# Kernel optimization log

Measured on AMD Instinct MI355X. Metric: run time of the kernel, lower is better.

Reference implementation:

```python
import jax, jax.numpy as jnp
import numpy as np

B, S, D, H = 4, 2048, 512, 8
DH = D // H


def setup_inputs() -> dict:
    key = jax.random.key(0)
    ks = jax.random.split(key, 7)
    scale = 1.0 / np.sqrt(DH)  # mimic nn.Linear init magnitude
    return {
        "x": jax.random.normal(ks[0], (B, S, D), dtype=jnp.float32),
        "Wq": jax.random.normal(ks[1], (H, DH, DH), dtype=jnp.float32) * scale,
        "bq": jax.random.normal(ks[2], (H, DH), dtype=jnp.float32) * scale,
        "Wk": jax.random.normal(ks[3], (H, DH, DH), dtype=jnp.float32) * scale,
        "bk": jax.random.normal(ks[4], (H, DH), dtype=jnp.float32) * scale,
        "Wv": jax.random.normal(ks[5], (H, DH, DH), dtype=jnp.float32) * scale,
        "bv": jax.random.normal(ks[6], (H, DH), dtype=jnp.float32) * scale,
    }


def reference(x, Wq, bq, Wk, bk, Wv, bv):
    # x: [B, S, D] -> per-head slices [B, S, H, DH] (contiguous chunks, as in torch slicing)
    xh = x.reshape(B, S, H, DH)
    # nn.Linear: y = x @ W.T + b, per head. Wq[h] is [out, in].
    q = jnp.einsum("bshd,hed->bshe", xh, Wq) + bq  # [B, S, H, DH]
    k = jnp.einsum("bshd,hed->bshe", xh, Wk) + bk
    v = jnp.einsum("bshd,hed->bshe", xh, Wv) + bv
    scores = jnp.einsum("bshe,bthe->bhst", q, k) / jnp.sqrt(jnp.float32(DH))  # [B, H, S, S]
    attn = jax.nn.softmax(scores, axis=-1)
    out = jnp.einsum("bhst,bthe->bshe", attn, v)  # [B, S, H, DH]
    return out.reshape(B, S, D)  # hstack of head outputs == concat along feature dim
```

## Files before the change

### kernel.cpp

```cpp
#include <hip/hip_runtime.h>
#include <math.h>

#define B_ 4
#define S_ 2048
#define D_ 512
#define H_ 8
#define DH_ 64
#define BH_ (B_*H_)
#define SCALE 0.1803368801111243f

typedef __attribute__((ext_vector_type(4))) float f32x4;
typedef __attribute__((ext_vector_type(8))) short bf16x8;

__device__ inline uint rnepk(float a, float b) {
    uint ua = __builtin_bit_cast(uint, a), ub = __builtin_bit_cast(uint, b);
    ua += 0x7FFFu + ((ua >> 16) & 1u);
    ub += 0x7FFFu + ((ub >> 16) & 1u);
    return (ua >> 16) | (ub & 0xFFFF0000u);
}
__device__ inline uint truncpk(float lo, float hi) {
    return __builtin_amdgcn_perm(__builtin_bit_cast(uint, hi),
                                 __builtin_bit_cast(uint, lo), 0x07060302u);
}

__global__ __launch_bounds__(256)
void qkv_mfma(const float* __restrict__ x,
              const float* __restrict__ Wq, const float* __restrict__ bq,
              const float* __restrict__ Wk, const float* __restrict__ bk,
              const float* __restrict__ Wv, const float* __restrict__ bv,
              ushort* __restrict__ Qb, ushort* __restrict__ Kb,
              ushort* __restrict__ Vtg)
{
    const int bh = blockIdx.x, b = bh >> 3, h = bh & 7;
    const int s0 = blockIdx.y * 64;
    const int tid = threadIdx.x;
    const int w = tid >> 6, lane = tid & 63, la = lane & 15, lg = lane >> 4;

    __shared__ __align__(16) ushort xs[64 * 64];
    __shared__ __align__(16) ushort wl[3 * 64 * 64];

    {
        const int s = tid >> 2, ch0 = (tid & 3) * 2;
        const float* xr = x + ((size_t)(b * S_ + s0 + s)) * D_ + h * DH_ + ch0 * 8;
        float4 f0 = *(const float4*)(xr);
        float4 f1 = *(const float4*)(xr + 4);
        float4 f2 = *(const float4*)(xr + 8);
        float4 f3 = *(const float4*)(xr + 12);
        uint4 c0, c1;
        c0.x = rnepk(f0.x, f0.y); c0.y = rnepk(f0.z, f0.w);
        c0.z = rnepk(f1.x, f1.y); c0.w = rnepk(f1.z, f1.w);
        c1.x = rnepk(f2.x, f2.y); c1.y = rnepk(f2.z, f2.w);
        c1.z = rnepk(f3.x, f3.y); c1.w = rnepk(f3.z, f3.w);
        *(uint4*)(xs + s * 64 + ((ch0 ^ (s & 7)) * 8)) = c0;
        *(uint4*)(xs + s * 64 + (((ch0 + 1) ^ (s & 7)) * 8)) = c1;
    }
    {
        const float* Wm[3] = {Wq, Wk, Wv};
        #pragma unroll
        for (int it = 0; it < 6; ++it) {
            const int mat = it >> 1;
            const int e = (it & 1) * 32 + (tid >> 3);
            const int ch = tid & 7;
            const float* p = Wm[mat] + h * DH_ * DH_ + e * DH_ + ch * 8;
            float4 a = *(const float4*)(p);
            float4 bb = *(const float4*)(p + 4);
            uint4 u;
            u.x = rnepk(a.x, a.y);  u.y = rnepk(a.z, a.w);
            u.z = rnepk(bb.x, bb.y); u.w = rnepk(bb.z, bb.w);
            *(uint4*)(wl + mat * 4096 + e * 64 + ((ch ^ (e & 7)) * 8)) = u;
        }
    }
    __syncthreads();

    const int srow = w * 16 + la;
    const ushort* xrow = xs + srow * 64;
    bf16x8 xf0 = *(const bf16x8*)(xrow + ((lg ^ (la & 7)) * 8));
    bf16x8 xf1 = *(const bf16x8*)(xrow + (((4 + lg) ^ (la & 7)) * 8));

    const size_t qkbase = ((size_t)(bh * S_ + s0 + srow)) * DH_;

    #pragma unroll
    for (int t4 = 0; t4 < 4; ++t4) {
        const int er = t4 * 16 + la;
        const ushort* wqr = wl + er * 64;
        const ushort* wkr = wl + 4096 + er * 64;
        const ushort* wvr = wl + 8192 + er * 64;
        const int c0 = (lg ^ (la & 7)) * 8, c1 = ((4 + lg) ^ (la & 7)) * 8;
        bf16x8 wq0 = *(const bf16x8*)(wqr + c0), wq1 = *(const bf16x8*)(wqr + c1);
        bf16x8 wk0 = *(const bf16x8*)(wkr + c0), wk1 = *(const bf16x8*)(wkr + c1);
        bf16x8 wv0 = *(const bf16x8*)(wvr + c0), wv1 = *(const bf16x8*)(wvr + c1);

        f32x4 aq = {0.f,0.f,0.f,0.f}, ak = {0.f,0.f,0.f,0.f}, av = {0.f,0.f,0.f,0.f};
        aq = __builtin_amdgcn_mfma_f32_16x16x32_bf16(wq0, xf0, aq, 0, 0, 0);
        aq = __builtin_amdgcn_mfma_f32_16x16x32_bf16(wq1, xf1, aq, 0, 0, 0);
        ak = __builtin_amdgcn_mfma_f32_16x16x32_bf16(wk0, xf0, ak, 0, 0, 0);
        ak = __builtin_amdgcn_mfma_f32_16x16x32_bf16(wk1, xf1, ak, 0, 0, 0);
        av = __builtin_amdgcn_mfma_f32_16x16x32_bf16(xf0, wv0, av, 0, 0, 0);
        av = __builtin_amdgcn_mfma_f32_16x16x32_bf16(xf1, wv1, av, 0, 0, 0);

        float4 bq4 = *(const float4*)(bq + h * DH_ + t4 * 16 + lg * 4);
        float4 bk4 = *(const float4*)(bk + h * DH_ + t4 * 16 + lg * 4);
        float bvv = bv[h * DH_ + er];

        uint2 qo, ko, vo;
        qo.x = rnepk((aq[0] + bq4.x) * SCALE, (aq[1] + bq4.y) * SCALE);
        qo.y = rnepk((aq[2] + bq4.z) * SCALE, (aq[3] + bq4.w) * SCALE);
        ko.x = rnepk(ak[0] + bk4.x, ak[1] + bk4.y);
        ko.y = rnepk(ak[2] + bk4.z, ak[3] + bk4.w);
        vo.x = rnepk(av[0] + bvv, av[1] + bvv);
        vo.y = rnepk(av[2] + bvv, av[3] + bvv);
        *(uint2*)(Qb + qkbase + t4 * 16 + lg * 4) = qo;
        *(uint2*)(Kb + qkbase + t4 * 16 + lg * 4) = ko;
        *(uint2*)(Vtg + ((size_t)(bh * DH_ + er)) * S_ + s0 + w * 16 + lg * 4) = vo;
    }
}

__global__ __launch_bounds__(256)
void flash_mfma(const ushort* __restrict__ Qb, const ushort* __restrict__ Kb,
                const ushort* __restrict__ Vtg, float* __restrict__ out)
{
    const int blk = blockIdx.x;
    const int bh = blk >> 5, qc = blk & 31;
    const int b = bh >> 3, h = bh & 7;
    const int tid = threadIdx.x;
    const int w = tid >> 6, lane = tid & 63, la = lane & 15, lg = lane >> 4;

    __shared__ __align__(16) ushort Ks[64 * 64];
    __shared__ __align__(16) ushort Vs[64 * 64];
    __shared__ __align__(16) ushort Ps[4][16 * 72];

    const int q0 = qc * 64 + w * 16;
    const ushort* qrow = Qb + ((size_t)(bh * S_) + q0 + la) * DH_;
    bf16x8 qf0 = *(const bf16x8*)(qrow + lg * 8);
    bf16x8 qf1 = *(const bf16x8*)(qrow + 32 + lg * 8);

    f32x4 O[4];
    #pragma unroll
    for (int t4 = 0; t4 < 4; ++t4) O[t4] = (f32x4){0.f, 0.f, 0.f, 0.f};
    float lsum = 0.f;

    const int sr = tid >> 3, sch = tid & 7;
    const ushort* kq = Kb + (size_t)bh * S_ * DH_ + (size_t)sr * DH_ + sch * 8;
    const ushort* vq = Vtg + (size_t)bh * DH_ * S_ + (size_t)sr * S_ + sch * 8;
    ushort* ksw = Ks + sr * 64 + ((sch ^ (sr & 7)) * 8);
    ushort* vsw = Vs + sr * 64 + ((sch ^ (sr & 7)) * 8);
    ushort* pw = &Ps[w][0];

    for (int kt = 0; kt < 32; ++kt) {
        __syncthreads();
        uint4 k0 = *(const uint4*)(kq);
        uint4 k1 = *(const uint4*)(kq + 32 * DH_);
        uint4 v0 = *(const uint4*)(vq);
        uint4 v1 = *(const uint4*)(vq + 32 * S_);
        *(uint4*)(ksw) = k0;
        *(uint4*)(ksw + 32 * 64) = k1;
        *(uint4*)(vsw) = v0;
        *(uint4*)(vsw + 32 * 64) = v1;
        __syncthreads();
        kq += 64 * DH_;
        vq += 64;

        f32x4 sc[4];
        #pragma unroll
        for (int t4 = 0; t4 < 4; ++t4) {
            const int r = t4 * 16 + la;
            bf16x8 a0 = *(const bf16x8*)(Ks + r * 64 + ((lg ^ (r & 7)) * 8));
            bf16x8 a1 = *(const bf16x8*)(Ks + r * 64 + (((4 + lg) ^ (r & 7)) * 8));
            f32x4 acc = {0.f, 0.f, 0.f, 0.f};
            acc = __builtin_amdgcn_mfma_f32_16x16x32_bf16(a0, qf0, acc, 0, 0, 0);
            acc = __builtin_amdgcn_mfma_f32_16x16x32_bf16(a1, qf1, acc, 0, 0, 0);
            sc[t4] = acc;
        }

        #pragma unroll
        for (int t4 = 0; t4 < 4; ++t4) {
            float p0 = __builtin_amdgcn_exp2f(sc[t4][0]);
            float p1 = __builtin_amdgcn_exp2f(sc[t4][1]);
            float p2 = __builtin_amdgcn_exp2f(sc[t4][2]);
            float p3 = __builtin_amdgcn_exp2f(sc[t4][3]);
            lsum += (p0 + p1) + (p2 + p3);
            uint2 pk;
            pk.x = truncpk(p0, p1);
            pk.y = truncpk(p2, p3);
            *(uint2*)(pw + la * 72 + t4 * 16 + lg * 4) = pk;
        }

        bf16x8 pa0 = *(const bf16x8*)(pw + la * 72 + lg * 8);
        bf16x8 pa1 = *(const bf16x8*)(pw + la * 72 + 32 + lg * 8);
        #pragma unroll
        for (int t4 = 0; t4 < 4; ++t4) {
            const int r = t4 * 16 + la;
            bf16x8 vb0 = *(const bf16x8*)(Vs + r * 64 + ((lg ^ (r & 7)) * 8));
            bf16x8 vb1 = *(const bf16x8*)(Vs + r * 64 + (((4 + lg) ^ (r & 7)) * 8));
            O[t4] = __builtin_amdgcn_mfma_f32_16x16x32_bf16(pa0, vb0, O[t4], 0, 0, 0);
            O[t4] = __builtin_amdgcn_mfma_f32_16x16x32_bf16(pa1, vb1, O[t4], 0, 0, 0);
        }
    }

    lsum += __shfl_xor(lsum, 16);
    lsum += __shfl_xor(lsum, 32);
    const float linv = 1.0f / lsum;

    float lr[4];
    #pragma unroll
    for (int r = 0; r < 4; ++r) lr[r] = __shfl(linv, lg * 4 + r);

    #pragma unroll
    for (int t4 = 0; t4 < 4; ++t4)
        #pragma unroll
        for (int r = 0; r < 4; ++r) {
            const int row = q0 + lg * 4 + r;
            out[((size_t)(b * S_) + row) * D_ + h * DH_ + t4 * 16 + la] = O[t4][r] * lr[r];
        }
}

extern "C" void kernel_launch(void* const* d_in, const int* in_sizes, int n_in,
                              void* d_out, int out_size, void* d_ws, size_t ws_size,
                              hipStream_t stream) {
    const float* x  = (const float*)d_in[0];
    const float* Wq = (const float*)d_in[1];
    const float* bq = (const float*)d_in[2];
    const float* Wk = (const float*)d_in[3];
    const float* bk = (const float*)d_in[4];
    const float* Wv = (const float*)d_in[5];
    const float* bv = (const float*)d_in[6];
    float* outp = (float*)d_out;

    ushort* Qb  = (ushort*)d_ws;
    ushort* Kb  = Qb + (size_t)BH_ * S_ * DH_;
    ushort* Vtg = Kb + (size_t)BH_ * S_ * DH_;

    qkv_mfma<<<dim3(BH_, S_ / 64), 256, 0, stream>>>(x, Wq, bq, Wk, bk, Wv, bv,
                                                     Qb, Kb, Vtg);
    flash_mfma<<<dim3(BH_ * 32), 256, 0, stream>>>(Qb, Kb, Vtg, outp);
}
```

Measured before the change: 143.3 us.

## Rewrite QKV and flash kernels with 32x32 MFMA tiles and double-buffered K/V

Both kernels move from 16x16x32 to 32x32x16 bf16 MFMA. In the flash kernel each wave now handles 64 query rows instead of 16, which raises K/V reuse per LDS load. K/V tiles are double-buffered in LDS, with global loads for the next tile issued before compute, and outputs are staged through LDS for coalesced stores. The QKV kernel processes 128 rows per block and also stages Q/K/V through LDS for coalesced writes. The flash grid shrinks to 256 blocks, which may underfill the GPU's compute units, and register pressure rises.

```diff
diff --git a/kernel.cpp b/kernel.cpp
--- a/kernel.cpp
+++ b/kernel.cpp
@@ -9,8 +9,9 @@
 #define BH_ (B_*H_)
 #define SCALE 0.1803368801111243f
 
-typedef __attribute__((ext_vector_type(4))) float f32x4;
-typedef __attribute__((ext_vector_type(8))) short bf16x8;
+typedef __attribute__((ext_vector_type(4)))  float f32x4;
+typedef __attribute__((ext_vector_type(16))) float f32x16;
+typedef __attribute__((ext_vector_type(8)))  short bf16x8;
 
 __device__ inline uint rnepk(float a, float b) {
     uint ua = __builtin_bit_cast(uint, a), ub = __builtin_bit_cast(uint, b);
@@ -22,8 +23,14 @@
     return __builtin_amdgcn_perm(__builtin_bit_cast(uint, hi),
                                  __builtin_bit_cast(uint, lo), 0x07060302u);
 }
-
-__global__ __launch_bounds__(256)
+__device__ inline f32x16 zero16() {
+    f32x16 z;
+    #pragma unroll
+    for (int i = 0; i < 16; ++i) z[i] = 0.f;
+    return z;
+}
+
+__global__ __launch_bounds__(256, 2)
 void qkv_mfma(const float* __restrict__ x,
               const float* __restrict__ Wq, const float* __restrict__ bq,
               const float* __restrict__ Wk, const float* __restrict__ bk,
@@ -32,186 +39,286 @@
               ushort* __restrict__ Vtg)
 {
     const int bh = blockIdx.x, b = bh >> 3, h = bh & 7;
-    const int s0 = blockIdx.y * 64;
+    const int s0 = blockIdx.y * 128;
     const int tid = threadIdx.x;
-    const int w = tid >> 6, lane = tid & 63, la = lane & 15, lg = lane >> 4;
-
-    __shared__ __align__(16) ushort xs[64 * 64];
-    __shared__ __align__(16) ushort wl[3 * 64 * 64];
+    const int w = tid >> 6, lane = tid & 63, l31 = lane & 31, l5 = lane >> 5;
+
+    __shared__ __align__(16) ushort xs[128 * 64];
+    __shared__ __align__(16) ushort wl[3][64 * 64];
+    __shared__ __align__(16) ushort bnc[4][2560];
 
     {
-        const int s = tid >> 2, ch0 = (tid & 3) * 2;
-        const float* xr = x + ((size_t)(b * S_ + s0 + s)) * D_ + h * DH_ + ch0 * 8;
-        float4 f0 = *(const float4*)(xr);
-        float4 f1 = *(const float4*)(xr + 4);
-        float4 f2 = *(const float4*)(xr + 8);
-        float4 f3 = *(const float4*)(xr + 12);
-        uint4 c0, c1;
-        c0.x = rnepk(f0.x, f0.y); c0.y = rnepk(f0.z, f0.w);
-        c0.z = rnepk(f1.x, f1.y); c0.w = rnepk(f1.z, f1.w);
-        c1.x = rnepk(f2.x, f2.y); c1.y = rnepk(f2.z, f2.w);
-        c1.z = rnepk(f3.x, f3.y); c1.w = rnepk(f3.z, f3.w);
-        *(uint4*)(xs + s * 64 + ((ch0 ^ (s & 7)) * 8)) = c0;
-        *(uint4*)(xs + s * 64 + (((ch0 + 1) ^ (s & 7)) * 8)) = c1;
+        const int row = tid >> 1, half = tid & 1;
+        const float* xr = x + ((size_t)(b * S_ + s0 + row)) * D_ + h * DH_ + half * 32;
+        ushort* dst = xs + row * 64;
+        #pragma unroll
+        for (int i = 0; i < 2; ++i) {
+            float4 f0 = *(const float4*)(xr + i * 16);
+            float4 f1 = *(const float4*)(xr + i * 16 + 4);
+            float4 f2 = *(const float4*)(xr + i * 16 + 8);
+            float4 f3 = *(const float4*)(xr + i * 16 + 12);
+            uint4 c0, c1;
+            c0.x = rnepk(f0.x, f0.y); c0.y = rnepk(f0.z, f0.w);
+            c0.z = rnepk(f1.x, f1.y); c0.w = rnepk(f1.z, f1.w);
+            c1.x = rnepk(f2.x, f2.y); c1.y = rnepk(f2.z, f2.w);
+            c1.z = rnepk(f3.x, f3.y); c1.w = rnepk(f3.z, f3.w);
+            const int ch0 = half * 4 + i * 2;
+            *(uint4*)(dst + ((ch0 ^ (row & 7)) * 8)) = c0;
+            *(uint4*)(dst + (((ch0 + 1) ^ (row & 7)) * 8)) = c1;
+        }
     }
     {
         const float* Wm[3] = {Wq, Wk, Wv};
         #pragma unroll
         for (int it = 0; it < 6; ++it) {
             const int mat = it >> 1;
-            const int e = (it & 1) * 32 + (tid >> 3);
-            const int ch = tid & 7;
+            const int e = (it & 1) * 32 + (tid >> 3), ch = tid & 7;
             const float* p = Wm[mat] + h * DH_ * DH_ + e * DH_ + ch * 8;
             float4 a = *(const float4*)(p);
-            float4 bb = *(const float4*)(p + 4);
+            float4 c = *(const float4*)(p + 4);
             uint4 u;
-            u.x = rnepk(a.x, a.y);  u.y = rnepk(a.z, a.w);
-            u.z = rnepk(bb.x, bb.y); u.w = rnepk(bb.z, bb.w);
-            *(uint4*)(wl + mat * 4096 + e * 64 + ((ch ^ (e & 7)) * 8)) = u;
+            u.x = rnepk(a.x, a.y); u.y = rnepk(a.z, a.w);
+            u.z = rnepk(c.x, c.y); u.w = rnepk(c.z, c.w);
+            *(uint4*)(&wl[mat][e * 64 + ((ch ^ (e & 7)) * 8)]) = u;
         }
     }
     __syncthreads();
 
-    const int srow = w * 16 + la;
-    const ushort* xrow = xs + srow * 64;
-    bf16x8 xf0 = *(const bf16x8*)(xrow + ((lg ^ (la & 7)) * 8));
-    bf16x8 xf1 = *(const bf16x8*)(xrow + (((4 + lg) ^ (la & 7)) * 8));
-
-    const size_t qkbase = ((size_t)(bh * S_ + s0 + srow)) * DH_;
-
-    #pragma unroll
-    for (int t4 = 0; t4 < 4; ++t4) {
-        const int er = t4 * 16 + la;
-        const ushort* wqr = wl + er * 64;
-        const ushort* wkr = wl + 4096 + er * 64;
-        const ushort* wvr = wl + 8192 + er * 64;
-        const int c0 = (lg ^ (la & 7)) * 8, c1 = ((4 + lg) ^ (la & 7)) * 8;
-        bf16x8 wq0 = *(const bf16x8*)(wqr + c0), wq1 = *(const bf16x8*)(wqr + c1);
-        bf16x8 wk0 = *(const bf16x8*)(wkr + c0), wk1 = *(const bf16x8*)(wkr + c1);
-        bf16x8 wv0 = *(const bf16x8*)(wvr + c0), wv1 = *(const bf16x8*)(wvr + c1);
-
-        f32x4 aq = {0.f,0.f,0.f,0.f}, ak = {0.f,0.f,0.f,0.f}, av = {0.f,0.f,0.f,0.f};
-        aq = __builtin_amdgcn_mfma_f32_16x16x32_bf16(wq0, xf0, aq, 0, 0, 0);
-        aq = __builtin_amdgcn_mfma_f32_16x16x32_bf16(wq1, xf1, aq, 0, 0, 0);
-        ak = __builtin_amdgcn_mfma_f32_16x16x32_bf16(wk0, xf0, ak, 0, 0, 0);
-        ak = __builtin_amdgcn_mfma_f32_16x16x32_bf16(wk1, xf1, ak, 0, 0, 0);
-        av = __builtin_amdgcn_mfma_f32_16x16x32_bf16(xf0, wv0, av, 0, 0, 0);
-        av = __builtin_amdgcn_mfma_f32_16x16x32_bf16(xf1, wv1, av, 0, 0, 0);
-
-        float4 bq4 = *(const float4*)(bq + h * DH_ + t4 * 16 + lg * 4);
-        float4 bk4 = *(const float4*)(bk + h * DH_ + t4 * 16 + lg * 4);
-        float bvv = bv[h * DH_ + er];
-
-        uint2 qo, ko, vo;
-        qo.x = rnepk((aq[0] + bq4.x) * SCALE, (aq[1] + bq4.y) * SCALE);
-        qo.y = rnepk((aq[2] + bq4.z) * SCALE, (aq[3] + bq4.w) * SCALE);
-        ko.x = rnepk(ak[0] + bk4.x, ak[1] + bk4.y);
-        ko.y = rnepk(ak[2] + bk4.z, ak[3] + bk4.w);
-        vo.x = rnepk(av[0] + bvv, av[1] + bvv);
-        vo.y = rnepk(av[2] + bvv, av[3] + bvv);
-        *(uint2*)(Qb + qkbase + t4 * 16 + lg * 4) = qo;
-        *(uint2*)(Kb + qkbase + t4 * 16 + lg * 4) = ko;
-        *(uint2*)(Vtg + ((size_t)(bh * DH_ + er)) * S_ + s0 + w * 16 + lg * 4) = vo;
-    }
-}
-
-__global__ __launch_bounds__(256)
+    const int srow = w * 32 + l31;
+    bf16x8 xf[4];
+    #pragma unroll
+    for (int st = 0; st < 4; ++st)
+        xf[st] = *(const bf16x8*)(xs + srow * 64 + (((st * 2 + l5) ^ (srow & 7)) * 8));
+
+    ushort* mybnc = &bnc[w][0];
+
+    #pragma unroll
+    for (int mat = 0; mat < 2; ++mat) {
+        const float* bias = mat ? bk : bq;
+        f32x16 acc[2];
+        #pragma unroll
+        for (int et = 0; et < 2; ++et) {
+            acc[et] = zero16();
+            const int e = et * 32 + l31;
+            #pragma unroll
+            for (int st = 0; st < 4; ++st) {
+                bf16x8 wf = *(const bf16x8*)(&wl[mat][e * 64 + (((st * 2 + l5) ^ (e & 7)) * 8)]);
+                acc[et] = __builtin_amdgcn_mfma_f32_32x32x16_bf16(wf, xf[st], acc[et], 0, 0, 0);
+            }
+        }
+        #pragma unroll
+        for (int et = 0; et < 2; ++et)
+            #pragma unroll
+            for (int rg = 0; rg < 4; ++rg) {
+                float4 b4 = *(const float4*)(bias + h * DH_ + et * 32 + rg * 8 + l5 * 4);
+                float v0 = acc[et][rg * 4 + 0] + b4.x;
+                float v1 = acc[et][rg * 4 + 1] + b4.y;
+                float v2 = acc[et][rg * 4 + 2] + b4.z;
+                float v3 = acc[et][rg * 4 + 3] + b4.w;
+                if (mat == 0) { v0 *= SCALE; v1 *= SCALE; v2 *= SCALE; v3 *= SCALE; }
+                uint2 pk;
+                pk.x = rnepk(v0, v1); pk.y = rnepk(v2, v3);
+                *(uint2*)(mybnc + l31 * 72 + et * 32 + rg * 8 + l5 * 4) = pk;
+            }
+        ushort* Og = mat ? Kb : Qb;
+        #pragma unroll
+        for (int i = 0; i < 4; ++i) {
+            const int slot = lane + 64 * i;
+            const int r = slot >> 3, c = slot & 7;
+            uint4 v = *(const uint4*)(mybnc + r * 72 + c * 8);
+            *(uint4*)(Og + ((size_t)(bh * S_ + s0 + w * 32 + r)) * DH_ + c * 8) = v;
+        }
+    }
+
+    {
+        f32x16 acc[2];
+        #pragma unroll
+        for (int et = 0; et < 2; ++et) {
+            acc[et] = zero16();
+            const int e = et * 32 + l31;
+            #pragma unroll
+            for (int st = 0; st < 4; ++st) {
+                bf16x8 wf = *(const bf16x8*)(&wl[2][e * 64 + (((st * 2 + l5) ^ (e & 7)) * 8)]);
+                acc[et] = __builtin_amdgcn_mfma_f32_32x32x16_bf16(xf[st], wf, acc[et], 0, 0, 0);
+            }
+        }
+        const float bvv0 = bv[h * DH_ + l31], bvv1 = bv[h * DH_ + 32 + l31];
+        #pragma unroll
+        for (int et = 0; et < 2; ++et) {
+            const float bb = et ? bvv1 : bvv0;
+            #pragma unroll
+            for (int rg = 0; rg < 4; ++rg) {
+                float v0 = acc[et][rg * 4 + 0] + bb;
+                float v1 = acc[et][rg * 4 + 1] + bb;
+                float v2 = acc[et][rg * 4 + 2] + bb;
+                float v3 = acc[et][rg * 4 + 3] + bb;
+                uint2 pk;
+                pk.x = rnepk(v0, v1); pk.y = rnepk(v2, v3);
+                *(uint2*)(mybnc + (et * 32 + l31) * 40 + rg * 8 + l5 * 4) = pk;
+            }
+        }
+        #pragma unroll
+        for (int i = 0; i < 4; ++i) {
+            const int slot = lane + 64 * i;
+            const int r = slot >> 2, c = slot & 3;
+            uint4 v = *(const uint4*)(mybnc + r * 40 + c * 8);
+            *(uint4*)(Vtg + ((size_t)(bh * DH_ + r)) * S_ + s0 + w * 32 + c * 8) = v;
+        }
+    }
+}
+
+__global__ __launch_bounds__(256, 1)
 void flash_mfma(const ushort* __restrict__ Qb, const ushort* __restrict__ Kb,
                 const ushort* __restrict__ Vtg, float* __restrict__ out)
 {
     const int blk = blockIdx.x;
-    const int bh = blk >> 5, qc = blk & 31;
+    const int bh = blk & 31, qblk = blk >> 5;
     const int b = bh >> 3, h = bh & 7;
     const int tid = threadIdx.x;
-    const int w = tid >> 6, lane = tid & 63, la = lane & 15, lg = lane >> 4;
-
-    __shared__ __align__(16) ushort Ks[64 * 64];
-    __shared__ __align__(16) ushort Vs[64 * 64];
-    __shared__ __align__(16) ushort Ps[4][16 * 72];
-
-    const int q0 = qc * 64 + w * 16;
-    const ushort* qrow = Qb + ((size_t)(bh * S_) + q0 + la) * DH_;
-    bf16x8 qf0 = *(const bf16x8*)(qrow + lg * 8);
-    bf16x8 qf1 = *(const bf16x8*)(qrow + 32 + lg * 8);
-
-    f32x4 O[4];
-    #pragma unroll
-    for (int t4 = 0; t4 < 4; ++t4) O[t4] = (f32x4){0.f, 0.f, 0.f, 0.f};
-    float lsum = 0.f;
-
-    const int sr = tid >> 3, sch = tid & 7;
-    const ushort* kq = Kb + (size_t)bh * S_ * DH_ + (size_t)sr * DH_ + sch * 8;
-    const ushort* vq = Vtg + (size_t)bh * DH_ * S_ + (size_t)sr * S_ + sch * 8;
-    ushort* ksw = Ks + sr * 64 + ((sch ^ (sr & 7)) * 8);
-    ushort* vsw = Vs + sr * 64 + ((sch ^ (sr & 7)) * 8);
-    ushort* pw = &Ps[w][0];
+    const int w = tid >> 6, lane = tid & 63, l31 = lane & 31, l5 = lane >> 5;
+
+    __shared__ __align__(16) ushort lds_u[16384 + 4 * 64 * 72];
+    ushort* Pw = lds_u + 16384 + w * (64 * 72);
+
+    const int q0 = qblk * 256 + w * 64;
+    bf16x8 qf[2][4];
+    #pragma unroll
+    for (int qt = 0; qt < 2; ++qt)
+        #pragma unroll
+        for (int st = 0; st < 4; ++st)
+            qf[qt][st] = *(const bf16x8*)(Qb + ((size_t)(bh * S_ + q0 + qt * 32 + l31)) * DH_
+                                          + st * 16 + l5 * 8);
+
+    f32x16 O[2][2];
+    #pragma unroll
+    for (int i = 0; i < 2; ++i)
+        #pragma unroll
+        for (int j = 0; j < 2; ++j) O[i][j] = zero16();
+    float lsum[2] = {0.f, 0.f};
+
+    const ushort* kg = Kb + (size_t)bh * S_ * DH_;
+    const ushort* vg = Vtg + (size_t)bh * DH_ * S_;
+    const int sr0 = tid >> 3, sc0 = tid & 7;
+    const int sr1 = (tid + 256) >> 3, sc1 = tid & 7;
+
+    uint4 kv0, kv1, vv0, vv1;
+    kv0 = *(const uint4*)(kg + (size_t)sr0 * DH_ + sc0 * 8);
+    kv1 = *(const uint4*)(kg + (size_t)sr1 * DH_ + sc1 * 8);
+    vv0 = *(const uint4*)(vg + (size_t)sr0 * S_ + sc0 * 8);
+    vv1 = *(const uint4*)(vg + (size_t)sr1 * S_ + sc1 * 8);
+    *(uint4*)(lds_u + sr0 * 64 + ((sc0 ^ (sr0 & 7)) * 8)) = kv0;
+    *(uint4*)(lds_u + sr1 * 64 + ((sc1 ^ (sr1 & 7)) * 8)) = kv1;
+    *(uint4*)(lds_u + 8192 + sr0 * 64 + ((sc0 ^ (sr0 & 7)) * 8)) = vv0;
+    *(uint4*)(lds_u + 8192 + sr1 * 64 + ((sc1 ^ (sr1 & 7)) * 8)) = vv1;
 
     for (int kt = 0; kt < 32; ++kt) {
         __syncthreads();
-        uint4 k0 = *(const uint4*)(kq);
-        uint4 k1 = *(const uint4*)(kq + 32 * DH_);
-        uint4 v0 = *(const uint4*)(vq);
-        uint4 v1 = *(const uint4*)(vq + 32 * S_);
-        *(uint4*)(ksw) = k0;
-        *(uint4*)(ksw + 32 * 64) = k1;
-        *(uint4*)(vsw) = v0;
-        *(uint4*)(vsw + 32 * 64) = v1;
-        __syncthreads();
-        kq += 64 * DH_;
-        vq += 64;
-
-        f32x4 sc[4];
-        #pragma unroll
-        for (int t4 = 0; t4 < 4; ++t4) {
-            const int r = t4 * 16 + la;
-            bf16x8 a0 = *(const bf16x8*)(Ks + r * 64 + ((lg ^ (r & 7)) * 8));
-            bf16x8 a1 = *(const bf16x8*)(Ks + r * 64 + (((4 + lg) ^ (r & 7)) * 8));
-            f32x4 acc = {0.f, 0.f, 0.f, 0.f};
-            acc = __builtin_amdgcn_mfma_f32_16x16x32_bf16(a0, qf0, acc, 0, 0, 0);
-            acc = __builtin_amdgcn_mfma_f32_16x16x32_bf16(a1, qf1, acc, 0, 0, 0);
-            sc[t4] = acc;
-        }
-
-        #pragma unroll
-        for (int t4 = 0; t4 < 4; ++t4) {
-            float p0 = __builtin_amdgcn_exp2f(sc[t4][0]);
-            float p1 = __builtin_amdgcn_exp2f(sc[t4][1]);
-            float p2 = __builtin_amdgcn_exp2f(sc[t4][2]);
-            float p3 = __builtin_amdgcn_exp2f(sc[t4][3]);
-            lsum += (p0 + p1) + (p2 + p3);
-            uint2 pk;
-            pk.x = truncpk(p0, p1);
-            pk.y = truncpk(p2, p3);
-            *(uint2*)(pw + la * 72 + t4 * 16 + lg * 4) = pk;
-        }
-
-        bf16x8 pa0 = *(const bf16x8*)(pw + la * 72 + lg * 8);
-        bf16x8 pa1 = *(const bf16x8*)(pw + la * 72 + 32 + lg * 8);
-        #pragma unroll
-        for (int t4 = 0; t4 < 4; ++t4) {
-            const int r = t4 * 16 + la;
-            bf16x8 vb0 = *(const bf16x8*)(Vs + r * 64 + ((lg ^ (r & 7)) * 8));
-            bf16x8 vb1 = *(const bf16x8*)(Vs + r * 64 + (((4 + lg) ^ (r & 7)) * 8));
-            O[t4] = __builtin_amdgcn_mfma_f32_16x16x32_bf16(pa0, vb0, O[t4], 0, 0, 0);
-            O[t4] = __builtin_amdgcn_mfma_f32_16x16x32_bf16(pa1, vb1, O[t4], 0, 0, 0);
-        }
-    }
-
-    lsum += __shfl_xor(lsum, 16);
-    lsum += __shfl_xor(lsum, 32);
-    const float linv = 1.0f / lsum;
-
-    float lr[4];
-    #pragma unroll
-    for (int r = 0; r < 4; ++r) lr[r] = __shfl(linv, lg * 4 + r);
-
-    #pragma unroll
-    for (int t4 = 0; t4 < 4; ++t4)
-        #pragma unroll
-        for (int r = 0; r < 4; ++r) {
-            const int row = q0 + lg * 4 + r;
-            out[((size_t)(b * S_) + row) * D_ + h * DH_ + t4 * 16 + la] = O[t4][r] * lr[r];
-        }
+        const int cur = kt & 1, nxt = cur ^ 1;
+        if (kt < 31) {
+            const size_t ko = (size_t)(kt + 1) * 64 * DH_;
+            const int vo = (kt + 1) * 64;
+            kv0 = *(const uint4*)(kg + ko + (size_t)sr0 * DH_ + sc0 * 8);
+            kv1 = *(const uint4*)(kg + ko + (size_t)sr1 * DH_ + sc1 * 8);
+            vv0 = *(const uint4*)(vg + (size_t)sr0 * S_ + vo + sc0 * 8);
+            vv1 = *(const uint4*)(vg + (size_t)sr1 * S_ + vo + sc1 * 8);
+        }
+        const ushort* ksb = lds_u + cur * 4096;
+        const ushort* vsb = lds_u + 8192 + cur * 4096;
+
+        #pragma unroll
+        for (int kt32 = 0; kt32 < 2; ++kt32) {
+            const int key = kt32 * 32 + l31;
+            bf16x8 kf[4];
+            #pragma unroll
+            for (int st = 0; st < 4; ++st)
+                kf[st] = *(const bf16x8*)(ksb + key * 64 + (((st * 2 + l5) ^ (key & 7)) * 8));
+            #pragma unroll
+            for (int qt = 0; qt < 2; ++qt) {
+                f32x16 sc = zero16();
+                #pragma unroll
+                for (int st = 0; st < 4; ++st)
+                    sc = __builtin_amdgcn_mfma_f32_32x32x16_bf16(kf[st], qf[qt][st], sc, 0, 0, 0);
+                float ls = 0.f;
+                #pragma unroll
+                for (int rg = 0; rg < 4; ++rg) {
+                    float p0 = __builtin_amdgcn_exp2f(sc[rg * 4 + 0]);
+                    float p1 = __builtin_amdgcn_exp2f(sc[rg * 4 + 1]);
+                    float p2 = __builtin_amdgcn_exp2f(sc[rg * 4 + 2]);
+                    float p3 = __builtin_amdgcn_exp2f(sc[rg * 4 + 3]);
+                    ls += (p0 + p1) + (p2 + p3);
+                    uint2 pk;
+                    pk.x = truncpk(p0, p1); pk.y = truncpk(p2, p3);
+                    *(uint2*)(Pw + (qt * 32 + l31) * 72 + kt32 * 32 + rg * 8 + l5 * 4) = pk;
+                }
+                lsum[qt] += ls;
+            }
+        }
+
+        bf16x8 pf[2][4];
+        #pragma unroll
+        for (int qt = 0; qt < 2; ++qt)
+            #pragma unroll
+            for (int st = 0; st < 4; ++st)
+                pf[qt][st] = *(const bf16x8*)(Pw + (qt * 32 + l31) * 72 + st * 16 + l5 * 8);
+        #pragma unroll
+        for (int dht = 0; dht < 2; ++dht) {
+            const int dh = dht * 32 + l31;
+            bf16x8 vf[4];
+            #pragma unroll
+            for (int st = 0; st < 4; ++st)
+                vf[st] = *(const bf16x8*)(vsb + dh * 64 + (((st * 2 + l5) ^ (dh & 7)) * 8));
+            #pragma unroll
+            for (int qt = 0; qt < 2; ++qt)
+                #pragma unroll
+                for (int st = 0; st < 4; ++st)
+                    O[dht][qt] = __builtin_amdgcn_mfma_f32_32x32x16_bf16(vf[st], pf[qt][st],
+                                                                          O[dht][qt], 0, 0, 0);
+        }
+
+        if (kt < 31) {
+            ushort* kn = lds_u + nxt * 4096;
+            ushort* vn = lds_u + 8192 + nxt * 4096;
+            *(uint4*)(kn + sr0 * 64 + ((sc0 ^ (sr0 & 7)) * 8)) = kv0;
+            *(uint4*)(kn + sr1 * 64 + ((sc1 ^ (sr1 & 7)) * 8)) = kv1;
+            *(uint4*)(vn + sr0 * 64 + ((sc0 ^ (sr0 & 7)) * 8)) = vv0;
+            *(uint4*)(vn + sr1 * 64 + ((sc1 ^ (sr1 & 7)) * 8)) = vv1;
+        }
+    }
+
+    #pragma unroll
+    for (int qt = 0; qt < 2; ++qt) {
+        float l = lsum[qt] + __shfl_xor(lsum[qt], 32);
+        lsum[qt] = 1.0f / l;
+    }
+    #pragma unroll
+    for (int dht = 0; dht < 2; ++dht)
+        #pragma unroll
+        for (int qt = 0; qt < 2; ++qt)
+            #pragma unroll
+            for (int i = 0; i < 16; ++i) O[dht][qt][i] *= lsum[qt];
+
+    __syncthreads();
+    float* ob = (float*)lds_u + w * (64 * 68);
+    #pragma unroll
+    for (int dht = 0; dht < 2; ++dht)
+        #pragma unroll
+        for (int qt = 0; qt < 2; ++qt)
+            #pragma unroll
+            for (int rg = 0; rg < 4; ++rg) {
+                f32x4 v4;
+                v4[0] = O[dht][qt][rg * 4 + 0];
+                v4[1] = O[dht][qt][rg * 4 + 1];
+                v4[2] = O[dht][qt][rg * 4 + 2];
+                v4[3] = O[dht][qt][rg * 4 + 3];
+                *(f32x4*)(ob + (qt * 32 + l31) * 68 + dht * 32 + rg * 8 + l5 * 4) = v4;
+            }
+    #pragma unroll
+    for (int i = 0; i < 16; ++i) {
+        const int slot = lane + 64 * i;
+        const int r = slot >> 4, c = slot & 15;
+        f32x4 v = *(const f32x4*)(ob + r * 68 + c * 4);
+        *(f32x4*)(out + ((size_t)(b * S_ + q0 + r)) * D_ + h * DH_ + c * 4) = v;
+    }
 }
 
 extern "C" void kernel_launch(void* const* d_in, const int* in_sizes, int n_in,
@@ -230,7 +337,7 @@
     ushort* Kb  = Qb + (size_t)BH_ * S_ * DH_;
     ushort* Vtg = Kb + (size_t)BH_ * S_ * DH_;
 
-    qkv_mfma<<<dim3(BH_, S_ / 64), 256, 0, stream>>>(x, Wq, bq, Wk, bk, Wv, bv,
-                                                     Qb, Kb, Vtg);
-    flash_mfma<<<dim3(BH_ * 32), 256, 0, stream>>>(Qb, Kb, Vtg, outp);
-}
+    qkv_mfma<<<dim3(BH_, S_ / 128), 256, 0, stream>>>(x, Wq, bq, Wk, bk, Wv, bv,
+                                                      Qb, Kb, Vtg);
+    flash_mfma<<<dim3(BH_ * 8), 256, 0, stream>>>(Qb, Kb, Vtg, outp);
+}
```

New measurement: 143.3 us. No clear change (+0.0%).
